# Kernel optimization log

Measured on AMD Instinct MI355X. Metric: run time of the kernel, lower is better.

The kernel has to match this reference:

```python
import jax, jax.numpy as jnp
import numpy as np

N = 20000        # nodes
E = 160000       # edges
MUL = 64         # multiplicity per irrep (0e and 1o)
EDIM = 8         # scalar edge-embedding dim (radial basis)
NZ = 4           # node-attr (species one-hot) channels
AVG_NEIGH = 8.0  # avg_num_neighbors
INV_SQRT3 = float(1.0 / np.sqrt(3.0))  # CG norm for 1o x 1o -> 0e


def setup_inputs() -> dict:
    key = jax.random.key(0)
    ks = jax.random.split(key, 13)
    s = lambda fan: 1.0 / np.sqrt(fan)
    return {
        "node_feats": jax.random.normal(ks[0], (N, 256), jnp.float32),          # 64x0e | 64x1o (flattened)
        "node_attrs": jax.random.uniform(ks[1], (N, NZ), jnp.float32),
        "edge_attrs": jax.random.normal(ks[2], (E, 4), jnp.float32),            # SH lmax=1: [Y0 | Y1(3)]
        "edge_embedding": jax.random.normal(ks[3], (E, EDIM), jnp.float32),
        # linear_1 (per-irrep channel mixing)
        "W_lin1_0": jax.random.normal(ks[4], (MUL, MUL), jnp.float32),
        "W_lin1_1": jax.random.normal(ks[5], (MUL, MUL), jnp.float32),
        # radial MLP: EDIM -> EDIM -> 4*MUL tp weights
        "W_mlp1": jax.random.normal(ks[6], (EDIM, EDIM), jnp.float32),
        "W_mlp2": jax.random.normal(ks[7], (EDIM, 4 * MUL), jnp.float32),
        # linear_2: 128x0e+128x1o -> 128x0e+64x1o
        "W_lin2_0": jax.random.normal(ks[8], (2 * MUL, 2 * MUL), jnp.float32),
        "W_lin2_1": jax.random.normal(ks[9], (2 * MUL, MUL), jnp.float32),
        # self-connection FCTP weights: (u, z, w)
        "W_sc0": jax.random.normal(ks[10], (MUL, NZ, 2 * MUL), jnp.float32),
        "W_sc1": jax.random.normal(ks[11], (MUL, NZ, MUL), jnp.float32),
        "edge_index": jax.random.randint(ks[12], (2, E), 0, N, dtype=jnp.int32),
    }


def reference(node_feats, node_attrs, edge_attrs, edge_embedding,
              W_lin1_0, W_lin1_1, W_mlp1, W_mlp2,
              W_lin2_0, W_lin2_1, W_sc0, W_sc1, edge_index):
    edge_src, edge_dst = edge_index[0], edge_index[1]

    # split node feats into irrep blocks: 64x0e scalars, 64x1o vectors
    x0 = node_feats[:, :MUL]                         # [N, 64]
    x1 = node_feats[:, MUL:].reshape(N, MUL, 3)      # [N, 64, 3]

    # linear_1 (e3nn Linear, per-irrep, 1/sqrt(fan_in))
    inv = 1.0 / np.sqrt(MUL)
    h0 = (x0 @ W_lin1_0) * inv                       # [N, 64]
    h1 = jnp.einsum("nud,uv->nvd", x1, W_lin1_1) * inv

    # radial MLP -> per-edge UVU weights (e3nn FullyConnectedNet: no bias, silu, 1/sqrt(fan_in))
    inv_e = 1.0 / np.sqrt(EDIM)
    hid = jax.nn.silu((edge_embedding @ W_mlp1) * inv_e)
    w = (hid @ W_mlp2) * inv_e                       # [E, 4*MUL]
    w1, w2, w3, w4 = w[:, :MUL], w[:, MUL:2*MUL], w[:, 2*MUL:3*MUL], w[:, 3*MUL:]

    # gather source-node features per edge
    g0 = h0[edge_src]                                # [E, 64]
    g1 = h1[edge_src]                                # [E, 64, 3]
    a0 = edge_attrs[:, :1]                           # [E, 1]  Y0
    a1 = edge_attrs[:, 1:]                           # [E, 3]  Y1

    # UVU tensor product paths (v = 1 for SH attrs)
    m0_a = w1 * g0 * a0                              # 0e x 0e -> 0e
    m0_b = w4 * jnp.einsum("eud,ed->eu", g1, a1) * INV_SQRT3   # 1o x 1o -> 0e
    m1_a = (w2 * g0)[:, :, None] * a1[:, None, :]    # 0e x 1o -> 1o
    m1_b = (w3[:, :, None] * g1) * a0[:, :, None]    # 1o x 0e -> 1o
    msg0 = jnp.concatenate([m0_a, m0_b], axis=1)     # [E, 128]
    msg1 = jnp.concatenate([m1_a, m1_b], axis=1)     # [E, 128, 3]

    # scatter_add to destination nodes, normalize by sqrt(avg_num_neighbors)
    inv_n = 1.0 / np.sqrt(AVG_NEIGH)
    s0 = jax.ops.segment_sum(msg0, edge_dst, num_segments=N) * inv_n   # [N, 128]
    s1 = jax.ops.segment_sum(msg1, edge_dst, num_segments=N) * inv_n   # [N, 128, 3]

    # linear_2: 128x0e+128x1o -> 128x0e (64 scalars + 64 gates) + 64x1o
    inv2 = 1.0 / np.sqrt(2 * MUL)
    u0 = (s0 @ W_lin2_0) * inv2                      # [N, 128]
    u1 = jnp.einsum("nud,uw->nwd", s1, W_lin2_1) * inv2   # [N, 64, 3]

    # self-connection FCTP with 0e node attrs (species-conditioned linear)
    inv_sc = 1.0 / np.sqrt(MUL * NZ)
    sc0 = jnp.einsum("nu,nz,uzw->nw", x0, node_attrs, W_sc0) * inv_sc
    sc1 = jnp.einsum("nud,nz,uzw->nwd", x1, node_attrs, W_sc1) * inv_sc
    t0 = u0 + sc0                                    # [N, 128]
    t1 = u1 + sc1                                    # [N, 64, 3]

    # Gate nonlinearity: silu on scalars, silu(gates) * vectors
    scalars = jax.nn.silu(t0[:, :MUL])               # [N, 64]
    gates = jax.nn.silu(t0[:, MUL:])                 # [N, 64]
    vectors = gates[:, :, None] * t1                 # [N, 64, 3]

    out = jnp.concatenate([scalars, vectors.reshape(N, MUL * 3)], axis=1)  # [N, 256]
    # resnet (irreps match input)
    return node_feats + out
```

## Files before the change

kernel.cpp:

```cpp
#include <hip/hip_runtime.h>
#include <hip/hip_bf16.h>
#include <math.h>

#define N 20000
#define E 160000
#define MUL 64
#define EDIM 8
#define NZ 4

#define INV_SQRT_MUL 0.125f
#define INV_E 0.35355339059327373f
#define INV_N 0.35355339059327373f
#define INV2 0.08838834764831845f
#define INV_SC 0.0625f
#define INV_SQRT3 0.5773502691896258f

typedef unsigned short u16;
typedef unsigned int u32;
typedef short bf16x8 __attribute__((ext_vector_type(8)));
typedef float f32x4 __attribute__((ext_vector_type(4)));

__device__ __forceinline__ float silu(float v) {
    return v / (1.0f + __expf(-v));
}
__device__ __forceinline__ u16 f2bf(float f) {
    union { float f; unsigned int u; } v; v.f = f;
    unsigned int r = (v.u + 0x7FFFu + ((v.u >> 16) & 1u)) >> 16;
    return (u16)r;
}
__device__ __forceinline__ float bflo(u32 p) {
    union { unsigned int u; float f; } v; v.u = p << 16; return v.f;
}
__device__ __forceinline__ float bfhi(u32 p) {
    union { unsigned int u; float f; } v; v.u = p & 0xFFFF0000u; return v.f;
}
#define MFMA(a, b, c) __builtin_amdgcn_mfma_f32_16x16x32_bf16(a, b, c, 0, 0, 0)


#define PREP_B  5000
#define WCONV_B 320
#define HID_B   5000
#define LIST_B  625

__global__ __launch_bounds__(256) void k_front(
    const float* __restrict__ x,
    const float* __restrict__ eemb, const int* __restrict__ eidx,
    const float* __restrict__ W20, const float* __restrict__ Wsc0,
    const float* __restrict__ W21, const float* __restrict__ Wsc1,
    const float* __restrict__ W0, const float* __restrict__ W1,
    const float* __restrict__ Wm1,
    u16* __restrict__ A1, u16* __restrict__ x1p,
    u16* __restrict__ Bt1m, u16* __restrict__ Bt1z, u16* __restrict__ Bt2,
    u16* __restrict__ W0b, u16* __restrict__ W1b,
    float* __restrict__ hid, int* __restrict__ head, int2* __restrict__ nl)
{
    const int b = blockIdx.x;
    const int tid = threadIdx.x;
    __shared__ float xr[4][256];

    if (b < PREP_B) {
        const int n0 = b * 4;
        #pragma unroll
        for (int t = 0; t < 4; ++t)
            xr[t][tid] = x[(size_t)(n0 + t) * 256 + tid];
        __syncthreads();
        #pragma unroll
        for (int t = 0; t < 4; ++t) {
            const int n = n0 + t;
            if (tid < 64) {
                A1[(size_t)n * 192 + 128 + tid] = f2bf(xr[t][tid]);
            } else {
                int q = tid - 64;
                int d = q >> 6, uu = q & 63;
                x1p[((size_t)n * 3 + d) * 64 + uu] = f2bf(xr[t][64 + uu * 3 + d]);
            }
        }
    } else if (b < PREP_B + WCONV_B) {
        int i = (b - PREP_B) * 256 + tid;
        if (i < 16384) {
            int w = i >> 7, k = i & 127;
            Bt1m[i] = f2bf(W20[k * 128 + w]);
        } else if (i < 49152) {
            int j = i - 16384;
            int z = j >> 13, r = j & 8191, w = r >> 6, k = r & 63;
            Bt1z[j] = f2bf(Wsc0[(k * 4 + z) * 128 + w] * INV_SC);
        } else if (i < 73728) {
            int j = i - 49152;
            int w = j / 384, k = j % 384;
            float v = (k < 128) ? W21[k * 64 + w] : Wsc1[(k - 128) * 64 + w];
            Bt2[j] = f2bf(v);
        } else if (i < 77824) {
            int j = i - 73728;
            int v = j >> 6, u = j & 63;
            W0b[j] = f2bf(W0[u * 64 + v] * INV_SQRT_MUL);
        } else {
            int j = i - 77824;
            int v = j >> 6, u = j & 63;
            W1b[j] = f2bf(W1[u * 64 + v] * INV_SQRT_MUL);
        }
    } else if (b < PREP_B + WCONV_B + HID_B) {
        int i = (b - PREP_B - WCONV_B) * 256 + tid;
        int e = i >> 3, k = i & 7;
        float s = 0.f;
        #pragma unroll
        for (int j = 0; j < 8; ++j)
            s += eemb[(size_t)e * 8 + j] * Wm1[j * 8 + k];
        hid[i] = silu(s * INV_E);
    } else {
        int e = (b - PREP_B - WCONV_B - HID_B) * 256 + tid;
        if (e < E) {
            int src = eidx[e];
            int dst = eidx[E + e];
            int old = atomicExch(&head[dst], e);
            nl[e] = make_int2(old, src);
        }
    }
}

__global__ __launch_bounds__(256) void k_hgemm(
    const u16* __restrict__ A1, const u16* __restrict__ x1p,
    const u16* __restrict__ W0b, const u16* __restrict__ W1b,
    u16* __restrict__ hc)
{
    const int lane = threadIdx.x & 63;
    const int g = blockIdx.x * 4 + (threadIdx.x >> 6);
    const int quad = lane >> 4, l16 = lane & 15;
    const bool isC1 = (g >= 1250);
    const int row0 = isC1 ? (g - 1250) * 16 : g * 16;
    const u16* Ap = isC1 ? (x1p + (size_t)(row0 + l16) * 64)
                         : (A1 + (size_t)(row0 + l16) * 192 + 128);
    const u16* Bp = isC1 ? W1b : W0b;

    f32x4 acc[4] = {};
    #pragma unroll
    for (int k0 = 0; k0 < 64; k0 += 32) {
        bf16x8 a = *(const bf16x8*)(Ap + k0 + quad * 8);
        #pragma unroll
        for (int ct = 0; ct < 4; ++ct) {
            bf16x8 bb = *(const bf16x8*)(Bp + (size_t)(ct * 16 + l16) * 64 + k0 + quad * 8);
            acc[ct] = MFMA(a, bb, acc[ct]);
        }
    }
    #pragma unroll
    for (int ct = 0; ct < 4; ++ct) {
        #pragma unroll
        for (int r = 0; r < 4; ++r) {
            int row = row0 + quad * 4 + r;
            int vv = ct * 16 + l16;
            if (!isC1) {
                hc[(size_t)row * 256 + vv * 4] = f2bf(acc[ct][r]);
            } else {
                int n = row / 3, d = row - 3 * (row / 3);
                hc[(size_t)n * 256 + vv * 4 + 1 + d] = f2bf(acc[ct][r]);
            }
        }
    }
}

__global__ __launch_bounds__(256) void k_gather(
    const int* __restrict__ head, const int2* __restrict__ nl,
    const float* __restrict__ eattr, const float* __restrict__ hid,
    const u32* __restrict__ hc2, const float* __restrict__ Wm2,
    u16* __restrict__ A1, u16* __restrict__ A2g)
{
    const int lane = threadIdx.x & 63;
    const int n = blockIdx.x * 4 + (threadIdx.x >> 6);

    float wm0[8], wm1[8], wm2r[8], wm3[8];
    #pragma unroll
    for (int k = 0; k < 8; ++k) {
        wm0[k]  = Wm2[k * 256 + lane];
        wm1[k]  = Wm2[k * 256 + 64 + lane];
        wm2r[k] = Wm2[k * 256 + 128 + lane];
        wm3[k]  = Wm2[k * 256 + 192 + lane];
    }

    float acc0a = 0.f, acc0b = 0.f;
    float s1a[3] = {0.f, 0.f, 0.f}, s1b[3] = {0.f, 0.f, 0.f};

    int e0 = head[n];
    if (e0 != -1) {
        int2 v0 = nl[e0];
        float4 ea = ((const float4*)eattr)[e0];
        float4 hA = ((const float4*)hid)[(size_t)e0 * 2];
        float4 hB = ((const float4*)hid)[(size_t)e0 * 2 + 1];
        uint2  hp = ((const uint2*)hc2)[(size_t)v0.y * 64 + lane];
        int e1 = v0.x;
        int2 v1 = make_int2(-1, 0);
        if (e1 != -1) v1 = nl[e1];

        while (true) {
            int e2 = -1;
            int2 v2 = make_int2(-1, 0);
            float4 eaN, hAN, hBN; uint2 hpN;
            if (e1 != -1) {
                e2 = v1.x;
                if (e2 != -1) v2 = nl[e2];
                eaN = ((const float4*)eattr)[e1];
                hAN = ((const float4*)hid)[(size_t)e1 * 2];
                hBN = ((const float4*)hid)[(size_t)e1 * 2 + 1];
                hpN = ((const uint2*)hc2)[(size_t)v1.y * 64 + lane];
            }

            float w1 = hA.x*wm0[0]+hA.y*wm0[1]+hA.z*wm0[2]+hA.w*wm0[3]
                     + hB.x*wm0[4]+hB.y*wm0[5]+hB.z*wm0[6]+hB.w*wm0[7];
            float w2 = hA.x*wm1[0]+hA.y*wm1[1]+hA.z*wm1[2]+hA.w*wm1[3]
                     + hB.x*wm1[4]+hB.y*wm1[5]+hB.z*wm1[6]+hB.w*wm1[7];
            float w3 = hA.x*wm2r[0]+hA.y*wm2r[1]+hA.z*wm2r[2]+hA.w*wm2r[3]
                     + hB.x*wm2r[4]+hB.y*wm2r[5]+hB.z*wm2r[6]+hB.w*wm2r[7];
            float w4 = hA.x*wm3[0]+hA.y*wm3[1]+hA.z*wm3[2]+hA.w*wm3[3]
                     + hB.x*wm3[4]+hB.y*wm3[5]+hB.z*wm3[6]+hB.w*wm3[7];
            const float g0 = bflo(hp.x), g1x = bfhi(hp.x);
            const float g1y = bflo(hp.y), g1z = bfhi(hp.y);
            acc0a += w1 * g0 * ea.x;
            acc0b += w4 * (g1x * ea.y + g1y * ea.z + g1z * ea.w);
            const float wg = w2 * g0, w3a = w3 * ea.x;
            s1a[0] += wg * ea.y;  s1a[1] += wg * ea.z;  s1a[2] += wg * ea.w;
            s1b[0] += w3a * g1x;  s1b[1] += w3a * g1y;  s1b[2] += w3a * g1z;

            if (e1 == -1) break;
            ea = eaN; hA = hAN; hB = hBN; hp = hpN;
            e1 = e2; v1 = v2;
        }
    }

    const float f = INV_E * INV_N * INV2;
    u16* a1p = &A1[(size_t)n * 192];
    a1p[lane]      = f2bf(acc0a * f);
    a1p[64 + lane] = f2bf(acc0b * f * INV_SQRT3);
    #pragma unroll
    for (int d = 0; d < 3; ++d) {
        u16* a2p = &A2g[((size_t)n * 3 + d) * 128];
        a2p[lane]      = f2bf(s1a[d] * f);
        a2p[64 + lane] = f2bf(s1b[d] * f);
    }
}

__global__ __launch_bounds__(256) void k_gemm_fused(
    const u16* __restrict__ A1, const u16* __restrict__ A2g,
    const u16* __restrict__ x1p,
    const u16* __restrict__ Bt1m, const u16* __restrict__ Bt1z,
    const u16* __restrict__ Bt2,
    const float* __restrict__ attrs, const float* __restrict__ x,
    float* __restrict__ out)
{
    const int lane = threadIdx.x & 63;
    const int wave = threadIdx.x >> 6;
    const int quad = lane >> 4, l16 = lane & 15;
    const int n0 = blockIdx.x * 16;

    __shared__ float st0[16][132];
    __shared__ float st1[48][68];
    __shared__ float sat[16][4];
    if (threadIdx.x < 64)
        sat[threadIdx.x >> 2][threadIdx.x & 3] =
            attrs[(size_t)(n0 + (threadIdx.x >> 2)) * 4 + (threadIdx.x & 3)];
    __syncthreads();

    float atv[3][4];
    #pragma unroll
    for (int rt = 0; rt < 3; ++rt) {
        const int ro = rt * 16 + l16;
        const int nn = (ro * 21846) >> 16;
        #pragma unroll
        for (int z = 0; z < 4; ++z) atv[rt][z] = sat[nn][z] * INV_SC;
    }

    const u16* a0p  = A1  + (size_t)(n0 + l16) * 192 + quad * 8;
    const u16* a1p  = A2g + (size_t)(3 * n0 + l16) * 128 + quad * 8;
    const u16* b0p  = Bt1m + (size_t)(wave * 16 + l16) * 128 + quad * 8;
    const u16* b1p  = Bt1m + (size_t)((wave + 4) * 16 + l16) * 128 + quad * 8;
    const u16* bz0p = Bt1z + (size_t)(wave * 16 + l16) * 64 + quad * 8;
    const u16* bz1p = Bt1z + (size_t)((wave + 4) * 16 + l16) * 64 + quad * 8;
    const u16* b2p  = Bt2 + (size_t)(wave * 16 + l16) * 384 + quad * 8;
    const u16* xq0  = x1p + (size_t)(3 * n0 + l16) * 64 + quad * 2;
    const u16* xq1  = x1p + (size_t)(3 * n0 + 16 + l16) * 64 + quad * 2;
    const u16* xq2  = x1p + (size_t)(3 * n0 + 32 + l16) * 64 + quad * 2;

    f32x4 m0 = {}, m1 = {};
    f32x4 mt[3] = {};
    f32x4 z0[4] = {}, z1[4] = {};

    #pragma unroll
    for (int kt = 0; kt < 4; ++kt) {
        const int ko = kt * 32;
        bf16x8 a1 = *(const bf16x8*)(a1p + ko);
        bf16x8 a2 = *(const bf16x8*)(a1p + 16 * 128 + ko);
        bf16x8 a3 = *(const bf16x8*)(a1p + 32 * 128 + ko);
        bf16x8 b2 = *(const bf16x8*)(b2p + ko);
        mt[0] = MFMA(a1, b2, mt[0]);
        mt[1] = MFMA(a2, b2, mt[1]);
        mt[2] = MFMA(a3, b2, mt[2]);
    }
    #pragma unroll
    for (int kt = 0; kt < 8; ++kt) {
        bf16x8 b2 = *(const bf16x8*)(b2p + 128 + kt * 32);
        const u32 xpa = *(const u32*)(xq0 + kt * 8);
        const u32 xpb = *(const u32*)(xq1 + kt * 8);
        const u32 xpc = *(const u32*)(xq2 + kt * 8);
        #pragma unroll
        for (int rt = 0; rt < 3; ++rt) {
            const u32 xp = (rt == 0) ? xpa : (rt == 1) ? xpb : xpc;
            const float xa = bflo(xp), xb = bfhi(xp);
            bf16x8 af;
            #pragma unroll
            for (int j = 0; j < 4; ++j) af[j] = (short)f2bf(xa * atv[rt][j]);
            #pragma unroll
            for (int j = 0; j < 4; ++j) af[4 + j] = (short)f2bf(xb * atv[rt][j]);
            mt[rt] = MFMA(af, b2, mt[rt]);
        }
    }
    #pragma unroll
    for (int kt = 0; kt < 4; ++kt) {
        const int ko = kt * 32;
        bf16x8 a0 = *(const bf16x8*)(a0p + ko);
        bf16x8 b0 = *(const bf16x8*)(b0p + ko);
        bf16x8 b1 = *(const bf16x8*)(b1p + ko);
        m0 = MFMA(a0, b0, m0);
        m1 = MFMA(a0, b1, m1);
    }
    #pragma unroll
    for (int kt = 0; kt < 2; ++kt) {
        const int ko = kt * 32;
        bf16x8 a0 = *(const bf16x8*)(a0p + 128 + ko);
        #pragma unroll
        for (int z = 0; z < 4; ++z) {
            bf16x8 c0 = *(const bf16x8*)(bz0p + z * 8192 + ko);
            bf16x8 c1 = *(const bf16x8*)(bz1p + z * 8192 + ko);
            z0[z] = MFMA(a0, c0, z0[z]);
            z1[z] = MFMA(a0, c1, z1[z]);
        }
    }
    __syncthreads();

    #pragma unroll
    for (int r = 0; r < 4; ++r) {
        const int r0 = quad * 4 + r;
        const float ta = sat[r0][0], tb = sat[r0][1],
                    tc = sat[r0][2], td = sat[r0][3];
        st0[r0][wave * 16 + l16] =
            m0[r] + ta * z0[0][r] + tb * z0[1][r] + tc * z0[2][r] + td * z0[3][r];
        st0[r0][(wave + 4) * 16 + l16] =
            m1[r] + ta * z1[0][r] + tb * z1[1][r] + tc * z1[2][r] + td * z1[3][r];
        st1[r0][wave * 16 + l16]      = mt[0][r];
        st1[16 + r0][wave * 16 + l16] = mt[1][r];
        st1[32 + r0][wave * 16 + l16] = mt[2][r];
    }
    __syncthreads();

    const int c = threadIdx.x;
    #pragma unroll
    for (int t = 0; t < 16; ++t) {
        const float xv = x[(size_t)(n0 + t) * 256 + c];
        float o;
        if (c < 64) {
            o = xv + silu(st0[t][c]);
        } else {
            int r = c - 64;
            int w = (r * 21846) >> 16;
            int d = r - w * 3;
            o = xv + silu(st0[t][64 + w]) * st1[t * 3 + d][w];
        }
        out[(size_t)(n0 + t) * 256 + c] = o;
    }
}

extern "C" void kernel_launch(void* const* d_in, const int* in_sizes, int n_in,
                              void* d_out, int out_size, void* d_ws, size_t ws_size,
                              hipStream_t stream) {
    const float* node_feats = (const float*)d_in[0];
    const float* node_attrs = (const float*)d_in[1];
    const float* edge_attrs = (const float*)d_in[2];
    const float* edge_emb   = (const float*)d_in[3];
    const float* W_lin1_0   = (const float*)d_in[4];
    const float* W_lin1_1   = (const float*)d_in[5];
    const float* W_mlp1     = (const float*)d_in[6];
    const float* W_mlp2     = (const float*)d_in[7];
    const float* W_lin2_0   = (const float*)d_in[8];
    const float* W_lin2_1   = (const float*)d_in[9];
    const float* W_sc0      = (const float*)d_in[10];
    const float* W_sc1      = (const float*)d_in[11];
    const int*   edge_index = (const int*)d_in[12];
    float* out = (float*)d_out;

    char* p = (char*)d_ws;
    float* hid = (float*)p;                 p += (size_t)E * 8 * 4;
    u16* hc    = (u16*)p;                   p += (size_t)N * 256 * 2;
    u16* A1    = (u16*)p;                   p += (size_t)N * 192 * 2;
    u16* A2g   = (u16*)p;                   p += (size_t)N * 3 * 128 * 2;
    u16* x1p   = (u16*)p;                   p += (size_t)N * 3 * 64 * 2;
    u16* Bt1m  = (u16*)p;                   p += 16384 * 2;
    u16* Bt1z  = (u16*)p;                   p += 32768 * 2;
    u16* Bt2   = (u16*)p;                   p += 24576 * 2;
    u16* W0b   = (u16*)p;                   p += 4096 * 2;
    u16* W1b   = (u16*)p;                   p += 4096 * 2;
    int* head  = (int*)p;                   p += N * 4;
    int2* nl   = (int2*)p;                  p += (size_t)E * 8;

    hipMemsetAsync(head, 0xFF, N * sizeof(int), stream);

    k_front<<<PREP_B + WCONV_B + HID_B + LIST_B, 256, 0, stream>>>(
        node_feats, edge_emb, edge_index,
        W_lin2_0, W_sc0, W_lin2_1, W_sc1, W_lin1_0, W_lin1_1, W_mlp1,
        A1, x1p, Bt1m, Bt1z, Bt2, W0b, W1b, hid, head, nl);
    k_hgemm<<<1250, 256, 0, stream>>>(A1, x1p, W0b, W1b, hc);
    k_gather<<<N / 4, 256, 0, stream>>>(head, nl, edge_attrs, hid,
                                        (const u32*)hc, W_mlp2, A1, A2g);
    k_gemm_fused<<<1250, 256, 0, stream>>>(A1, A2g, x1p, Bt1m, Bt1z, Bt2,
                                           node_attrs, node_feats, out);
}
```

Baseline: 213.5 us.

## Split fused output GEMM into specialized scalar and vector waves

The final fused GEMM kernel goes from 4 to 8 waves per block. Four waves compute the scalar path (linear_2 scalars plus the species-conditioned self-connection) and four compute the vector path, where before every wave did both serially. The residual input is now prefetched into registers before the barrier, one barrier and the shared attrs staging are dropped, and node attrs are read directly as float4. This aims to shorten each wave's dependent MFMA chain and hide the output-stage load latency, at the cost of a larger block and different register pressure under the new launch bounds.

```diff
diff --git a/kernel.cpp b/kernel.cpp
--- a/kernel.cpp
+++ b/kernel.cpp
@@ -236,7 +236,7 @@
     }
 }
 
-__global__ __launch_bounds__(256) void k_gemm_fused(
+__global__ __launch_bounds__(512, 8) void k_gemm_fused(
     const u16* __restrict__ A1, const u16* __restrict__ A2g,
     const u16* __restrict__ x1p,
     const u16* __restrict__ Bt1m, const u16* __restrict__ Bt1z,
@@ -248,118 +248,124 @@
     const int wave = threadIdx.x >> 6;
     const int quad = lane >> 4, l16 = lane & 15;
     const int n0 = blockIdx.x * 16;
+    const float4* at4 = (const float4*)attrs;
 
     __shared__ float st0[16][132];
     __shared__ float st1[48][68];
-    __shared__ float sat[16][4];
-    if (threadIdx.x < 64)
-        sat[threadIdx.x >> 2][threadIdx.x & 3] =
-            attrs[(size_t)(n0 + (threadIdx.x >> 2)) * 4 + (threadIdx.x & 3)];
+
+    if (wave < 4) {
+        const u16* a0p  = A1   + (size_t)(n0 + l16) * 192 + quad * 8;
+        const u16* b0p  = Bt1m + (size_t)(wave * 16 + l16) * 128 + quad * 8;
+        const u16* b1p  = Bt1m + (size_t)((wave + 4) * 16 + l16) * 128 + quad * 8;
+        const u16* bz0p = Bt1z + (size_t)(wave * 16 + l16) * 64 + quad * 8;
+        const u16* bz1p = Bt1z + (size_t)((wave + 4) * 16 + l16) * 64 + quad * 8;
+
+        f32x4 m0 = {}, m1 = {};
+        f32x4 z0[4] = {}, z1[4] = {};
+
+        #pragma unroll
+        for (int kt = 0; kt < 4; ++kt) {
+            bf16x8 a0 = *(const bf16x8*)(a0p + kt * 32);
+            bf16x8 b0 = *(const bf16x8*)(b0p + kt * 32);
+            bf16x8 b1 = *(const bf16x8*)(b1p + kt * 32);
+            m0 = MFMA(a0, b0, m0);
+            m1 = MFMA(a0, b1, m1);
+        }
+        #pragma unroll
+        for (int kt = 0; kt < 2; ++kt) {
+            bf16x8 a0 = *(const bf16x8*)(a0p + 128 + kt * 32);
+            #pragma unroll
+            for (int z = 0; z < 4; ++z) {
+                bf16x8 c0 = *(const bf16x8*)(bz0p + z * 8192 + kt * 32);
+                bf16x8 c1 = *(const bf16x8*)(bz1p + z * 8192 + kt * 32);
+                z0[z] = MFMA(a0, c0, z0[z]);
+                z1[z] = MFMA(a0, c1, z1[z]);
+            }
+        }
+
+        #pragma unroll
+        for (int r = 0; r < 4; ++r) {
+            const int r0 = quad * 4 + r;
+            const float4 a = at4[n0 + r0];
+            st0[r0][wave * 16 + l16] =
+                m0[r] + a.x * z0[0][r] + a.y * z0[1][r] + a.z * z0[2][r] + a.w * z0[3][r];
+            st0[r0][(wave + 4) * 16 + l16] =
+                m1[r] + a.x * z1[0][r] + a.y * z1[1][r] + a.z * z1[2][r] + a.w * z1[3][r];
+        }
+    } else {
+        const int ct = wave - 4;
+        const u16* a1p = A2g + (size_t)(3 * n0 + l16) * 128 + quad * 8;
+        const u16* b2p = Bt2 + (size_t)(ct * 16 + l16) * 384 + quad * 8;
+        const u16* xq0 = x1p + (size_t)(3 * n0 + l16) * 64 + quad * 2;
+
+        float4 atv[3];
+        #pragma unroll
+        for (int rt = 0; rt < 3; ++rt) {
+            const int ro = rt * 16 + l16;
+            const int nn = (ro * 21846) >> 16;
+            const float4 v = at4[n0 + nn];
+            atv[rt].x = v.x * INV_SC; atv[rt].y = v.y * INV_SC;
+            atv[rt].z = v.z * INV_SC; atv[rt].w = v.w * INV_SC;
+        }
+
+        f32x4 mt[3] = {};
+
+        #pragma unroll
+        for (int kt = 0; kt < 4; ++kt) {
+            const int ko = kt * 32;
+            bf16x8 b2 = *(const bf16x8*)(b2p + ko);
+            bf16x8 a1 = *(const bf16x8*)(a1p + ko);
+            bf16x8 a2 = *(const bf16x8*)(a1p + 16 * 128 + ko);
+            bf16x8 a3 = *(const bf16x8*)(a1p + 32 * 128 + ko);
+            mt[0] = MFMA(a1, b2, mt[0]);
+            mt[1] = MFMA(a2, b2, mt[1]);
+            mt[2] = MFMA(a3, b2, mt[2]);
+        }
+        #pragma unroll
+        for (int kt = 0; kt < 8; ++kt) {
+            bf16x8 b2 = *(const bf16x8*)(b2p + 128 + kt * 32);
+            #pragma unroll
+            for (int rt = 0; rt < 3; ++rt) {
+                const u32 xp = *(const u32*)(xq0 + rt * 16 * 64 + kt * 8);
+                const float xa = bflo(xp), xb = bfhi(xp);
+                bf16x8 af;
+                af[0] = (short)f2bf(xa * atv[rt].x); af[1] = (short)f2bf(xa * atv[rt].y);
+                af[2] = (short)f2bf(xa * atv[rt].z); af[3] = (short)f2bf(xa * atv[rt].w);
+                af[4] = (short)f2bf(xb * atv[rt].x); af[5] = (short)f2bf(xb * atv[rt].y);
+                af[6] = (short)f2bf(xb * atv[rt].z); af[7] = (short)f2bf(xb * atv[rt].w);
+                mt[rt] = MFMA(af, b2, mt[rt]);
+            }
+        }
+
+        #pragma unroll
+        for (int r = 0; r < 4; ++r) {
+            const int r0 = quad * 4 + r;
+            st1[r0][ct * 16 + l16]      = mt[0][r];
+            st1[16 + r0][ct * 16 + l16] = mt[1][r];
+            st1[32 + r0][ct * 16 + l16] = mt[2][r];
+        }
+    }
+
+    const int c = threadIdx.x & 255;
+    const int th = threadIdx.x >> 8;
+    float xv[8];
+    #pragma unroll
+    for (int i = 0; i < 8; ++i)
+        xv[i] = x[(size_t)(n0 + i * 2 + th) * 256 + c];
+
     __syncthreads();
 
-    float atv[3][4];
-    #pragma unroll
-    for (int rt = 0; rt < 3; ++rt) {
-        const int ro = rt * 16 + l16;
-        const int nn = (ro * 21846) >> 16;
-        #pragma unroll
-        for (int z = 0; z < 4; ++z) atv[rt][z] = sat[nn][z] * INV_SC;
-    }
-
-    const u16* a0p  = A1  + (size_t)(n0 + l16) * 192 + quad * 8;
-    const u16* a1p  = A2g + (size_t)(3 * n0 + l16) * 128 + quad * 8;
-    const u16* b0p  = Bt1m + (size_t)(wave * 16 + l16) * 128 + quad * 8;
-    const u16* b1p  = Bt1m + (size_t)((wave + 4) * 16 + l16) * 128 + quad * 8;
-    const u16* bz0p = Bt1z + (size_t)(wave * 16 + l16) * 64 + quad * 8;
-    const u16* bz1p = Bt1z + (size_t)((wave + 4) * 16 + l16) * 64 + quad * 8;
-    const u16* b2p  = Bt2 + (size_t)(wave * 16 + l16) * 384 + quad * 8;
-    const u16* xq0  = x1p + (size_t)(3 * n0 + l16) * 64 + quad * 2;
-    const u16* xq1  = x1p + (size_t)(3 * n0 + 16 + l16) * 64 + quad * 2;
-    const u16* xq2  = x1p + (size_t)(3 * n0 + 32 + l16) * 64 + quad * 2;
-
-    f32x4 m0 = {}, m1 = {};
-    f32x4 mt[3] = {};
-    f32x4 z0[4] = {}, z1[4] = {};
-
-    #pragma unroll
-    for (int kt = 0; kt < 4; ++kt) {
-        const int ko = kt * 32;
-        bf16x8 a1 = *(const bf16x8*)(a1p + ko);
-        bf16x8 a2 = *(const bf16x8*)(a1p + 16 * 128 + ko);
-        bf16x8 a3 = *(const bf16x8*)(a1p + 32 * 128 + ko);
-        bf16x8 b2 = *(const bf16x8*)(b2p + ko);
-        mt[0] = MFMA(a1, b2, mt[0]);
-        mt[1] = MFMA(a2, b2, mt[1]);
-        mt[2] = MFMA(a3, b2, mt[2]);
-    }
-    #pragma unroll
-    for (int kt = 0; kt < 8; ++kt) {
-        bf16x8 b2 = *(const bf16x8*)(b2p + 128 + kt * 32);
-        const u32 xpa = *(const u32*)(xq0 + kt * 8);
-        const u32 xpb = *(const u32*)(xq1 + kt * 8);
-        const u32 xpc = *(const u32*)(xq2 + kt * 8);
-        #pragma unroll
-        for (int rt = 0; rt < 3; ++rt) {
-            const u32 xp = (rt == 0) ? xpa : (rt == 1) ? xpb : xpc;
-            const float xa = bflo(xp), xb = bfhi(xp);
-            bf16x8 af;
-            #pragma unroll
-            for (int j = 0; j < 4; ++j) af[j] = (short)f2bf(xa * atv[rt][j]);
-            #pragma unroll
-            for (int j = 0; j < 4; ++j) af[4 + j] = (short)f2bf(xb * atv[rt][j]);
-            mt[rt] = MFMA(af, b2, mt[rt]);
-        }
-    }
-    #pragma unroll
-    for (int kt = 0; kt < 4; ++kt) {
-        const int ko = kt * 32;
-        bf16x8 a0 = *(const bf16x8*)(a0p + ko);
-        bf16x8 b0 = *(const bf16x8*)(b0p + ko);
-        bf16x8 b1 = *(const bf16x8*)(b1p + ko);
-        m0 = MFMA(a0, b0, m0);
-        m1 = MFMA(a0, b1, m1);
-    }
-    #pragma unroll
-    for (int kt = 0; kt < 2; ++kt) {
-        const int ko = kt * 32;
-        bf16x8 a0 = *(const bf16x8*)(a0p + 128 + ko);
-        #pragma unroll
-        for (int z = 0; z < 4; ++z) {
-            bf16x8 c0 = *(const bf16x8*)(bz0p + z * 8192 + ko);
-            bf16x8 c1 = *(const bf16x8*)(bz1p + z * 8192 + ko);
-            z0[z] = MFMA(a0, c0, z0[z]);
-            z1[z] = MFMA(a0, c1, z1[z]);
-        }
-    }
-    __syncthreads();
-
-    #pragma unroll
-    for (int r = 0; r < 4; ++r) {
-        const int r0 = quad * 4 + r;
-        const float ta = sat[r0][0], tb = sat[r0][1],
-                    tc = sat[r0][2], td = sat[r0][3];
-        st0[r0][wave * 16 + l16] =
-            m0[r] + ta * z0[0][r] + tb * z0[1][r] + tc * z0[2][r] + td * z0[3][r];
-        st0[r0][(wave + 4) * 16 + l16] =
-            m1[r] + ta * z1[0][r] + tb * z1[1][r] + tc * z1[2][r] + td * z1[3][r];
-        st1[r0][wave * 16 + l16]      = mt[0][r];
-        st1[16 + r0][wave * 16 + l16] = mt[1][r];
-        st1[32 + r0][wave * 16 + l16] = mt[2][r];
-    }
-    __syncthreads();
-
-    const int c = threadIdx.x;
-    #pragma unroll
-    for (int t = 0; t < 16; ++t) {
-        const float xv = x[(size_t)(n0 + t) * 256 + c];
+    #pragma unroll
+    for (int i = 0; i < 8; ++i) {
+        const int t = i * 2 + th;
         float o;
         if (c < 64) {
-            o = xv + silu(st0[t][c]);
+            o = xv[i] + silu(st0[t][c]);
         } else {
             int r = c - 64;
             int w = (r * 21846) >> 16;
             int d = r - w * 3;
-            o = xv + silu(st0[t][64 + w]) * st1[t * 3 + d][w];
+            o = xv[i] + silu(st0[t][64 + w]) * st1[t * 3 + d][w];
         }
         out[(size_t)(n0 + t) * 256 + c] = o;
     }
@@ -406,6 +412,6 @@
     k_hgemm<<<1250, 256, 0, stream>>>(A1, x1p, W0b, W1b, hc);
     k_gather<<<N / 4, 256, 0, stream>>>(head, nl, edge_attrs, hid,
                                         (const u32*)hc, W_mlp2, A1, A2g);
-    k_gemm_fused<<<1250, 256, 0, stream>>>(A1, A2g, x1p, Bt1m, Bt1z, Bt2,
+    k_gemm_fused<<<1250, 512, 0, stream>>>(A1, A2g, x1p, Bt1m, Bt1z, Bt2,
                                            node_attrs, node_feats, out);
 }
```

New measurement: 212.5 us. Within noise of the previous version (-0.5%).
